# Optimization experiments

Hardware: AMD Instinct MI355X
Metric: run time of the kernel (lower is better)

Reference implementation:

```python
import jax, jax.numpy as jnp
import numpy as np

N_NODES = 50000
N_EDGES = 800000
IN_CH = 128
HID = 64
HEADS = 4
OUT_CH = 1
NEG_SLOPE = 0.2  # PyG GATConv default


def setup_inputs() -> dict:
    key = jax.random.key(0)
    ks = jax.random.split(key, 16)
    s = 0.1
    x = jax.random.normal(ks[0], (N_NODES, IN_CH), dtype=jnp.float32)
    edge_index = jax.random.randint(ks[1], (2, N_EDGES), 0, N_NODES, dtype=jnp.int64)
    # GATConv 1: in=128 -> 64 per head, 4 heads, concat
    W1 = jax.random.normal(ks[2], (IN_CH, HEADS * HID), dtype=jnp.float32) * s
    att_src1 = jax.random.normal(ks[3], (HEADS, HID), dtype=jnp.float32) * s
    att_dst1 = jax.random.normal(ks[4], (HEADS, HID), dtype=jnp.float32) * s
    b1 = jnp.zeros((HEADS * HID,), dtype=jnp.float32)
    # GATConv 2: in=256 -> 64, 1 head, mean (concat=False)
    W2 = jax.random.normal(ks[5], (HEADS * HID, HID), dtype=jnp.float32) * s
    att_src2 = jax.random.normal(ks[6], (1, HID), dtype=jnp.float32) * s
    att_dst2 = jax.random.normal(ks[7], (1, HID), dtype=jnp.float32) * s
    b2 = jnp.zeros((HID,), dtype=jnp.float32)
    # MLP: Linear(128,64) -> ReLU -> Linear(64,1)
    mlp_w1 = jax.random.normal(ks[8], (2 * HID, HID), dtype=jnp.float32) * s
    mlp_b1 = jnp.zeros((HID,), dtype=jnp.float32)
    mlp_w2 = jax.random.normal(ks[9], (HID, OUT_CH), dtype=jnp.float32) * s
    mlp_b2 = jnp.zeros((OUT_CH,), dtype=jnp.float32)
    return dict(x=x, edge_index=edge_index, W1=W1, att_src1=att_src1,
                att_dst1=att_dst1, b1=b1, W2=W2, att_src2=att_src2,
                att_dst2=att_dst2, b2=b2, mlp_w1=mlp_w1, mlp_b1=mlp_b1,
                mlp_w2=mlp_w2, mlp_b2=mlp_b2)


def gat_layer(x, edge_index, W, att_src, att_dst, bias, heads, ch, concat):
    N = x.shape[0]
    # add self loops (PyG default add_self_loops=True)
    loop = jnp.arange(N, dtype=edge_index.dtype)
    src = jnp.concatenate([edge_index[0], loop])
    dst = jnp.concatenate([edge_index[1], loop])
    h = (x @ W).reshape(N, heads, ch)                      # [N,H,C]
    a_src = jnp.einsum('nhc,hc->nh', h, att_src)           # [N,H]
    a_dst = jnp.einsum('nhc,hc->nh', h, att_dst)
    logits = jax.nn.leaky_relu(a_src[src] + a_dst[dst], NEG_SLOPE)  # [E,H]
    # segment softmax over destination node
    m = jax.ops.segment_max(logits, dst, num_segments=N)
    e = jnp.exp(logits - m[dst])
    denom = jax.ops.segment_sum(e, dst, num_segments=N)
    alpha = e / denom[dst]                                 # [E,H]
    msg = alpha[:, :, None] * h[src]                       # [E,H,C]
    out = jax.ops.segment_sum(msg, dst, num_segments=N)    # [N,H,C]
    out = out.reshape(N, heads * ch) if concat else out.mean(axis=1)
    return out + bias


def reference(x, edge_index, W1, att_src1, att_dst1, b1,
              W2, att_src2, att_dst2, b2,
              mlp_w1, mlp_b1, mlp_w2, mlp_b2):
    # eval mode: dropouts are identity
    h = gat_layer(x, edge_index, W1, att_src1, att_dst1, b1, HEADS, HID, True)
    h = jax.nn.elu(h)
    h = gat_layer(h, edge_index, W2, att_src2, att_dst2, b2, 1, HID, False)
    u = h[edge_index[0]]                                   # [E,HID]
    v = h[edge_index[1]]
    ef = jnp.concatenate([u, v], axis=1)                   # [E,2*HID]
    hid = jax.nn.relu(ef @ mlp_w1 + mlp_b1)
    return hid @ mlp_w2 + mlp_b2                           # [E,OUT_CH]
```

## Files before the change

kernel.cpp:

```cpp
#include <hip/hip_runtime.h>
#include <hip/hip_bf16.h>
#include <math.h>

#define NN 50000
#define NE 800000
#define NB ((NN + 255) / 256)
#define NEG 0.2f

typedef __hip_bfloat16 bf16;
typedef __attribute__((ext_vector_type(8))) short s8v;
typedef __attribute__((ext_vector_type(4))) float f4v;

__device__ __forceinline__ float bf2f(unsigned short u) {
  union { unsigned int i; float f; } c;
  c.i = ((unsigned int)u) << 16;
  return c.f;
}
__device__ __forceinline__ float blo(unsigned int u) {
  union { unsigned int i; float f; } c;
  c.i = u << 16;
  return c.f;
}
__device__ __forceinline__ float bhi(unsigned int u) {
  union { unsigned int i; float f; } c;
  c.i = u & 0xffff0000u;
  return c.f;
}
__device__ __forceinline__ unsigned short f2b(float f) {
  bf16 b = __float2bfloat16(f);
  return __builtin_bit_cast(unsigned short, b);
}
__device__ __forceinline__ float lrelu(float t) { return (t > 0.f) ? t : NEG * t; }

__global__ void hist_k(const int* __restrict__ ei, int* __restrict__ counts) {
  int e = blockIdx.x * 256 + threadIdx.x;
  if (e >= NE) return;
  atomicAdd(&counts[ei[NE + e]], 1);
}

__global__ __launch_bounds__(256) void scan_bsum_k(const int* __restrict__ counts,
                                                   int* __restrict__ bsums) {
  __shared__ int wsum[4];
  int i = blockIdx.x * 256 + threadIdx.x;
  int v = (i < NN) ? counts[i] : 0;
#pragma unroll
  for (int off = 32; off; off >>= 1) v += __shfl_xor(v, off);
  if ((threadIdx.x & 63) == 0) wsum[threadIdx.x >> 6] = v;
  __syncthreads();
  if (threadIdx.x == 0) bsums[blockIdx.x] = wsum[0] + wsum[1] + wsum[2] + wsum[3];
}

__global__ __launch_bounds__(256) void scan_final_k(const int* __restrict__ counts,
                                                    const int* __restrict__ bsums,
                                                    int* __restrict__ offsets,
                                                    int* __restrict__ cursor) {
  __shared__ int s[256];
  __shared__ int wsum[4];
  __shared__ int bpref;
  int t = threadIdx.x;
  int bv = (t < NB && t < (int)blockIdx.x) ? bsums[t] : 0;
#pragma unroll
  for (int off = 32; off; off >>= 1) bv += __shfl_xor(bv, off);
  if ((t & 63) == 0) wsum[t >> 6] = bv;
  __syncthreads();
  if (t == 0) bpref = wsum[0] + wsum[1] + wsum[2] + wsum[3];
  int i = blockIdx.x * 256 + t;
  int v = (i < NN) ? counts[i] : 0;
  s[t] = v;
  __syncthreads();
  for (int off = 1; off < 256; off <<= 1) {
    int u = (t >= off) ? s[t - off] : 0;
    __syncthreads();
    s[t] += u;
    __syncthreads();
  }
  int excl = s[t] - v + bpref;
  if (i < NN) {
    offsets[i] = excl;
    cursor[i] = excl;
    if (i == NN - 1) offsets[NN] = excl + v;
  }
}

__global__ void scatter_k(const int* __restrict__ ei, int* __restrict__ cursor,
                          int2* __restrict__ csr) {
  int e = blockIdx.x * 256 + threadIdx.x;
  if (e >= NE) return;
  int s = ei[e], d = ei[NE + e];
  int pos = atomicAdd(&cursor[d], 1);
  csr[pos] = make_int2(s, e);
}

#define NX4 (NN * 32)
#define NW1 (256 * 128)
#define NW2 (64 * 256)
#define NPQ (128 * 64)
__global__ void conv_all_k(const float* __restrict__ x, const float* __restrict__ W1,
                           const float* __restrict__ W2, const float* __restrict__ mw1,
                           unsigned short* __restrict__ xb, unsigned short* __restrict__ w1t,
                           unsigned short* __restrict__ w2t, unsigned short* __restrict__ pqt) {
  int i = blockIdx.x * 256 + threadIdx.x;
  if (i < NX4) {
    float4 v = *(const float4*)(x + (size_t)i * 4);
    ushort4 o = {f2b(v.x), f2b(v.y), f2b(v.z), f2b(v.w)};
    *(ushort4*)(xb + (size_t)i * 4) = o;
    return;
  }
  i -= NX4;
  if (i < NW1) {
    int n = i >> 7, k = i & 127;
    w1t[i] = f2b(W1[(size_t)k * 256 + n]);
    return;
  }
  i -= NW1;
  if (i < NW2) {
    int n = i >> 8, k = i & 255;
    w2t[i] = f2b(W2[(size_t)k * 64 + n]);
    return;
  }
  i -= NW2;
  if (i < NPQ) {
    int n = i >> 6, k = i & 63;
    float v = (n < 64) ? mw1[(size_t)k * 64 + n] : mw1[(size_t)(64 + k) * 64 + (n - 64)];
    pqt[i] = f2b(v);
  }
}

template <int DOTS>
__global__ __launch_bounds__(256) void mgemm_k(
    const unsigned short* __restrict__ A, int lda,
    const unsigned short* __restrict__ Bt, int ldb,
    unsigned short* __restrict__ C, int ldc,
    int M, int N, int K,
    const float* __restrict__ ws, const float* __restrict__ wd,
    float* __restrict__ as_, float* __restrict__ ad_, int H) {
  __shared__ unsigned short Asl[64][40];
  __shared__ unsigned short Btl[64][40];
  __shared__ float sdot[64], ddot[64];
  int bm = blockIdx.y * 64, bn = blockIdx.x * 64;
  int t = threadIdx.x;
  int wv = t >> 6, lane = t & 63;
  int wm = (wv >> 1) * 32, wn = (wv & 1) * 32;
  int l16 = lane & 15, lq = lane >> 4;
  if (DOTS && t < 64) { sdot[t] = 0.f; ddot[t] = 0.f; }
  f4v acc[2][2];
#pragma unroll
  for (int mi = 0; mi < 2; ++mi)
#pragma unroll
    for (int ni = 0; ni < 2; ++ni) {
      acc[mi][ni][0] = 0.f; acc[mi][ni][1] = 0.f;
      acc[mi][ni][2] = 0.f; acc[mi][ni][3] = 0.f;
    }
  int sr = t >> 2, sc = (t & 3) * 8;
  for (int k0 = 0; k0 < K; k0 += 32) {
    uint4 av = {0, 0, 0, 0};
    int gr = bm + sr;
    if (gr < M) av = *(const uint4*)(A + (size_t)gr * lda + k0 + sc);
    *(uint4*)&Asl[sr][sc] = av;
    uint4 bv = *(const uint4*)(Bt + (size_t)(bn + sr) * ldb + k0 + sc);
    *(uint4*)&Btl[sr][sc] = bv;
    __syncthreads();
    s8v af[2], bfv[2];
#pragma unroll
    for (int mi = 0; mi < 2; ++mi)
      af[mi] = *(const s8v*)&Asl[wm + mi * 16 + l16][lq * 8];
#pragma unroll
    for (int ni = 0; ni < 2; ++ni)
      bfv[ni] = *(const s8v*)&Btl[wn + ni * 16 + l16][lq * 8];
#pragma unroll
    for (int mi = 0; mi < 2; ++mi)
#pragma unroll
      for (int ni = 0; ni < 2; ++ni)
        acc[mi][ni] = __builtin_amdgcn_mfma_f32_16x16x32_bf16(
            af[mi], bfv[ni], acc[mi][ni], 0, 0, 0);
    __syncthreads();
  }
#pragma unroll
  for (int mi = 0; mi < 2; ++mi)
#pragma unroll
    for (int rr = 0; rr < 4; ++rr) {
      int row = bm + wm + mi * 16 + lq * 4 + rr;
      if (row < M) {
#pragma unroll
        for (int ni = 0; ni < 2; ++ni) {
          int col = bn + wn + ni * 16 + l16;
          C[(size_t)row * ldc + col] = f2b(acc[mi][ni][rr]);
        }
      }
    }
  if (DOTS) {
    int head = blockIdx.x;
    float ps[2][4], pd[2][4];
#pragma unroll
    for (int mi = 0; mi < 2; ++mi)
#pragma unroll
      for (int rr = 0; rr < 4; ++rr) {
        float s = 0.f, d = 0.f;
#pragma unroll
        for (int ni = 0; ni < 2; ++ni) {
          int col = wn + ni * 16 + l16;
          s += acc[mi][ni][rr] * ws[head * 64 + col];
          d += acc[mi][ni][rr] * wd[head * 64 + col];
        }
        ps[mi][rr] = s;
        pd[mi][rr] = d;
      }
#pragma unroll
    for (int off = 1; off < 16; off <<= 1)
#pragma unroll
      for (int mi = 0; mi < 2; ++mi)
#pragma unroll
        for (int rr = 0; rr < 4; ++rr) {
          ps[mi][rr] += __shfl_xor(ps[mi][rr], off);
          pd[mi][rr] += __shfl_xor(pd[mi][rr], off);
        }
    if (l16 == 0) {
#pragma unroll
      for (int mi = 0; mi < 2; ++mi)
#pragma unroll
        for (int rr = 0; rr < 4; ++rr) {
          int rl = wm + mi * 16 + lq * 4 + rr;
          atomicAdd(&sdot[rl], ps[mi][rr]);
          atomicAdd(&ddot[rl], pd[mi][rr]);
        }
    }
    __syncthreads();
    if (t < 64 && bm + t < M) {
      as_[(size_t)(bm + t) * H + head] = sdot[t];
      ad_[(size_t)(bm + t) * H + head] = ddot[t];
    }
  }
}

__global__ __launch_bounds__(256) void gat_agg4_k(
    const int* __restrict__ offsets, const int2* __restrict__ csr,
    const unsigned short* __restrict__ h, const float* __restrict__ as_,
    const float* __restrict__ ad_, const float* __restrict__ bias,
    unsigned short* __restrict__ out) {
  __shared__ float exs[4][64][4];
  __shared__ int srcs[4][64];
  int wvx = threadIdx.x >> 6, lane = threadIdx.x & 63;
  int n = blockIdx.x * 4 + wvx;
  int hd = lane >> 4;
  int beg = offsets[n], end = offsets[n + 1];
  float4 adn = *(const float4*)(ad_ + (size_t)n * 4);
  float4 asn = *(const float4*)(as_ + (size_t)n * 4);
  float es0 = __expf(lrelu(asn.x + adn.x));
  float es1 = __expf(lrelu(asn.y + adn.y));
  float es2 = __expf(lrelu(asn.z + adn.z));
  float es3 = __expf(lrelu(asn.w + adn.w));
  float d0 = es0, d1 = es1, d2 = es2, d3 = es3;
  float wself = (hd == 0) ? es0 : (hd == 1) ? es1 : (hd == 2) ? es2 : es3;
  uint2 sv = *(const uint2*)(h + (size_t)n * 256 + lane * 4);
  float2 a01, a23;
  a01.x = wself * blo(sv.x); a01.y = wself * bhi(sv.x);
  a23.x = wself * blo(sv.y); a23.y = wself * bhi(sv.y);
  for (int base = beg; base < end; base += 64) {
    int cnt = min(64, end - base);
    int src = 0;
    float e0 = 0.f, e1 = 0.f, e2 = 0.f, e3 = 0.f;
    if (lane < cnt) {
      src = csr[base + lane].x;
      float4 a4 = *(const float4*)(as_ + (size_t)src * 4);
      e0 = __expf(lrelu(a4.x + adn.x));
      e1 = __expf(lrelu(a4.y + adn.y));
      e2 = __expf(lrelu(a4.z + adn.z));
      e3 = __expf(lrelu(a4.w + adn.w));
    }
    float s0 = e0, s1 = e1, s2 = e2, s3 = e3;
#pragma unroll
    for (int off = 32; off; off >>= 1) {
      s0 += __shfl_xor(s0, off);
      s1 += __shfl_xor(s1, off);
      s2 += __shfl_xor(s2, off);
      s3 += __shfl_xor(s3, off);
    }
    d0 += s0; d1 += s1; d2 += s2; d3 += s3;
    float4 ex4 = {e0, e1, e2, e3};
    *(float4*)(&exs[wvx][lane][0]) = ex4;
    srcs[wvx][lane] = src;
    __builtin_amdgcn_wave_barrier();
    int e = 0;
    for (; e + 16 <= cnt; e += 16) {
      uint2 r[16];
#pragma unroll
      for (int j = 0; j < 16; ++j)
        r[j] = *(const uint2*)(h + (size_t)srcs[wvx][e + j] * 256 + lane * 4);
#pragma unroll
      for (int j = 0; j < 16; ++j) {
        float w = exs[wvx][e + j][hd];
        a01.x += w * blo(r[j].x); a01.y += w * bhi(r[j].x);
        a23.x += w * blo(r[j].y); a23.y += w * bhi(r[j].y);
      }
    }
    for (; e + 4 <= cnt; e += 4) {
      uint2 r[4];
#pragma unroll
      for (int j = 0; j < 4; ++j)
        r[j] = *(const uint2*)(h + (size_t)srcs[wvx][e + j] * 256 + lane * 4);
#pragma unroll
      for (int j = 0; j < 4; ++j) {
        float w = exs[wvx][e + j][hd];
        a01.x += w * blo(r[j].x); a01.y += w * bhi(r[j].x);
        a23.x += w * blo(r[j].y); a23.y += w * bhi(r[j].y);
      }
    }
    for (; e < cnt; ++e) {
      int si = srcs[wvx][e];
      float w = exs[wvx][e][hd];
      uint2 r = *(const uint2*)(h + (size_t)si * 256 + lane * 4);
      a01.x += w * blo(r.x); a01.y += w * bhi(r.x);
      a23.x += w * blo(r.y); a23.y += w * bhi(r.y);
    }
  }
  float myden = (hd == 0) ? d0 : (hd == 1) ? d1 : (hd == 2) ? d2 : d3;
  float inv = 1.f / myden;
  float4 b4 = *(const float4*)(bias + lane * 4);
  float4 res;
  res.x = a01.x * inv + b4.x;
  res.y = a01.y * inv + b4.y;
  res.z = a23.x * inv + b4.z;
  res.w = a23.y * inv + b4.w;
  res.x = (res.x > 0.f) ? res.x : (__expf(res.x) - 1.f);
  res.y = (res.y > 0.f) ? res.y : (__expf(res.y) - 1.f);
  res.z = (res.z > 0.f) ? res.z : (__expf(res.z) - 1.f);
  res.w = (res.w > 0.f) ? res.w : (__expf(res.w) - 1.f);
  ushort4 ov = {f2b(res.x), f2b(res.y), f2b(res.z), f2b(res.w)};
  *(ushort4*)(out + (size_t)n * 256 + lane * 4) = ov;
}

__global__ __launch_bounds__(256) void gat_agg1_k(
    const int* __restrict__ offsets, const int2* __restrict__ csr,
    const unsigned short* __restrict__ h, const float* __restrict__ as_,
    const float* __restrict__ ad_, const float* __restrict__ bias,
    unsigned short* __restrict__ out) {
  __shared__ float exs[4][64];
  __shared__ int srcs[4][64];
  int wvx = threadIdx.x >> 6, lane = threadIdx.x & 63;
  int n = blockIdx.x * 4 + wvx;
  int slot = lane >> 4, cp = lane & 15;
  int beg = offsets[n], end = offsets[n + 1];
  float adn = ad_[n];
  float eself = __expf(lrelu(as_[n] + adn));
  float den = eself;
  float2 a01 = {0.f, 0.f}, a23 = {0.f, 0.f};
  if (slot == 0) {
    uint2 sv = *(const uint2*)(h + (size_t)n * 64 + cp * 4);
    a01.x = eself * blo(sv.x); a01.y = eself * bhi(sv.x);
    a23.x = eself * blo(sv.y); a23.y = eself * bhi(sv.y);
  }
  for (int base = beg; base < end; base += 64) {
    int cnt = min(64, end - base);
    int src = 0;
    float ex = 0.f;
    if (lane < cnt) {
      src = csr[base + lane].x;
      ex = __expf(lrelu(as_[src] + adn));
    }
    float s = ex;
#pragma unroll
    for (int off = 32; off; off >>= 1) s += __shfl_xor(s, off);
    den += s;
    exs[wvx][lane] = ex;
    srcs[wvx][lane] = src;
    __builtin_amdgcn_wave_barrier();
    int i = slot;
    for (; i + 12 < cnt; i += 16) {
      uint2 r[4];
      int i0 = i, i1 = i + 4, i2 = i + 8, i3 = i + 12;
      r[0] = *(const uint2*)(h + (size_t)srcs[wvx][i0] * 64 + cp * 4);
      r[1] = *(const uint2*)(h + (size_t)srcs[wvx][i1] * 64 + cp * 4);
      r[2] = *(const uint2*)(h + (size_t)srcs[wvx][i2] * 64 + cp * 4);
      r[3] = *(const uint2*)(h + (size_t)srcs[wvx][i3] * 64 + cp * 4);
      float w0 = exs[wvx][i0], w1 = exs[wvx][i1], w2 = exs[wvx][i2], w3 = exs[wvx][i3];
      a01.x += w0 * blo(r[0].x); a01.y += w0 * bhi(r[0].x);
      a23.x += w0 * blo(r[0].y); a23.y += w0 * bhi(r[0].y);
      a01.x += w1 * blo(r[1].x); a01.y += w1 * bhi(r[1].x);
      a23.x += w1 * blo(r[1].y); a23.y += w1 * bhi(r[1].y);
      a01.x += w2 * blo(r[2].x); a01.y += w2 * bhi(r[2].x);
      a23.x += w2 * blo(r[2].y); a23.y += w2 * bhi(r[2].y);
      a01.x += w3 * blo(r[3].x); a01.y += w3 * bhi(r[3].x);
      a23.x += w3 * blo(r[3].y); a23.y += w3 * bhi(r[3].y);
    }
    for (; i < cnt; i += 4) {
      int si = srcs[wvx][i];
      float w = exs[wvx][i];
      uint2 r = *(const uint2*)(h + (size_t)si * 64 + cp * 4);
      a01.x += w * blo(r.x); a01.y += w * bhi(r.x);
      a23.x += w * blo(r.y); a23.y += w * bhi(r.y);
    }
  }
#pragma unroll
  for (int off = 16; off <= 32; off <<= 1) {
    a01.x += __shfl_xor(a01.x, off);
    a01.y += __shfl_xor(a01.y, off);
    a23.x += __shfl_xor(a23.x, off);
    a23.y += __shfl_xor(a23.y, off);
  }
  if (slot == 0) {
    float inv = 1.f / den;
    float4 b4 = *(const float4*)(bias + cp * 4);
    ushort4 ov;
    ov.x = f2b(a01.x * inv + b4.x);
    ov.y = f2b(a01.y * inv + b4.y);
    ov.z = f2b(a23.x * inv + b4.z);
    ov.w = f2b(a23.y * inv + b4.w);
    *(ushort4*)(out + (size_t)n * 64 + cp * 4) = ov;
  }
}

__global__ __launch_bounds__(256) void edge_out_k(
    const int* __restrict__ offsets, const int2* __restrict__ csr,
    const unsigned short* __restrict__ pq,
    const float* __restrict__ mb1, const float* __restrict__ w2,
    const float* __restrict__ mb2, float* __restrict__ out) {
  int wvx = threadIdx.x >> 6, lane = threadIdx.x & 63;
  int n = blockIdx.x * 4 + wvx;
  int slot = lane >> 4, cp = lane & 15;
  int beg = offsets[n], end = offsets[n + 1];
  ushort4 qv = *(const ushort4*)(pq + (size_t)n * 128 + 64 + cp * 4);
  float4 base4 = *(const float4*)(mb1 + cp * 4);
  base4.x += bf2f(qv.x); base4.y += bf2f(qv.y);
  base4.z += bf2f(qv.z); base4.w += bf2f(qv.w);
  float4 w4 = *(const float4*)(w2 + cp * 4);
  float b2v = mb2[0];
  for (int base = beg; base < end; base += 4) {
    int i = base + slot;
    int2 se = {0, 0};
    bool ok = (i < end);
    if (ok) se = csr[i];
    float r = 0.f;
    if (ok) {
      ushort4 pv = *(const ushort4*)(pq + (size_t)se.x * 128 + cp * 4);
      float v0 = fmaxf(bf2f(pv.x) + base4.x, 0.f);
      float v1 = fmaxf(bf2f(pv.y) + base4.y, 0.f);
      float v2 = fmaxf(bf2f(pv.z) + base4.z, 0.f);
      float v3 = fmaxf(bf2f(pv.w) + base4.w, 0.f);
      r = v0 * w4.x + v1 * w4.y + v2 * w4.z + v3 * w4.w;
    }
    r += __shfl_xor(r, 8);
    r += __shfl_xor(r, 4);
    r += __shfl_xor(r, 2);
    r += __shfl_xor(r, 1);
    if (cp == 0 && ok) out[se.y] = r + b2v;
  }
}

extern "C" void kernel_launch(void* const* d_in, const int* in_sizes, int n_in,
                              void* d_out, int out_size, void* d_ws, size_t ws_size,
                              hipStream_t stream) {
  const float* x = (const float*)d_in[0];
  const int* ei = (const int*)d_in[1];
  const float* W1 = (const float*)d_in[2];
  const float* as1w = (const float*)d_in[3];
  const float* ad1w = (const float*)d_in[4];
  const float* b1 = (const float*)d_in[5];
  const float* W2 = (const float*)d_in[6];
  const float* as2w = (const float*)d_in[7];
  const float* ad2w = (const float*)d_in[8];
  const float* b2 = (const float*)d_in[9];
  const float* mw1 = (const float*)d_in[10];
  const float* mb1 = (const float*)d_in[11];
  const float* mw2 = (const float*)d_in[12];
  const float* mb2 = (const float*)d_in[13];
  float* out = (float*)d_out;

  char* ws = (char*)d_ws;
  size_t o = 0;
  auto alloc = [&](size_t bytes) {
    void* ptr = ws + o;
    o += (bytes + 255) & ~(size_t)255;
    return ptr;
  };
  int* counts = (int*)alloc((size_t)NN * 4);
  int* offsets = (int*)alloc((size_t)(NN + 1) * 4);
  int* cursor = (int*)alloc((size_t)NN * 4);
  int* bsums = (int*)alloc((size_t)NB * 4);
  int2* csr = (int2*)alloc((size_t)NE * 8);
  unsigned short* xb = (unsigned short*)alloc((size_t)NN * 128 * 2);
  unsigned short* w1t = (unsigned short*)alloc((size_t)256 * 128 * 2);
  unsigned short* w2t = (unsigned short*)alloc((size_t)64 * 256 * 2);
  unsigned short* pqt = (unsigned short*)alloc((size_t)128 * 64 * 2);
  unsigned short* h1b = (unsigned short*)alloc((size_t)NN * 256 * 2);
  float* a_s1 = (float*)alloc((size_t)NN * 4 * 4);
  float* a_d1 = (float*)alloc((size_t)NN * 4 * 4);
  unsigned short* x2b = (unsigned short*)alloc((size_t)NN * 256 * 2);
  unsigned short* yb = (unsigned short*)alloc((size_t)NN * 64 * 2);
  unsigned short* h2b = h1b;
  unsigned short* pq = h1b + (size_t)NN * 64;

  hipMemsetAsync(counts, 0, (size_t)NN * 4, stream);
  hist_k<<<(NE + 255) / 256, 256, 0, stream>>>(ei, counts);
  scan_bsum_k<<<NB, 256, 0, stream>>>(counts, bsums);
  scan_final_k<<<NB, 256, 0, stream>>>(counts, bsums, offsets, cursor);
  scatter_k<<<(NE + 255) / 256, 256, 0, stream>>>(ei, cursor, csr);

  conv_all_k<<<(NX4 + NW1 + NW2 + NPQ + 255) / 256, 256, 0, stream>>>(
      x, W1, W2, mw1, xb, w1t, w2t, pqt);

  int gy = (NN + 63) / 64;
  mgemm_k<1><<<dim3(4, gy), 256, 0, stream>>>(xb, 128, w1t, 128, h1b, 256,
                                              NN, 256, 128, as1w, ad1w, a_s1, a_d1, 4);
  gat_agg4_k<<<NN / 4, 256, 0, stream>>>(offsets, csr, h1b, a_s1, a_d1, b1, x2b);

  mgemm_k<1><<<dim3(1, gy), 256, 0, stream>>>(x2b, 256, w2t, 256, h2b, 64,
                                              NN, 64, 256, as2w, ad2w, a_s1, a_d1, 1);
  gat_agg1_k<<<NN / 4, 256, 0, stream>>>(offsets, csr, h2b, a_s1, a_d1, b2, yb);

  mgemm_k<0><<<dim3(2, gy), 256, 0, stream>>>(yb, 64, pqt, 64, pq, 128,
                                              NN, 128, 64, nullptr, nullptr,
                                              nullptr, nullptr, 0);

  edge_out_k<<<NN / 4, 256, 0, stream>>>(offsets, csr, pq, mb1, mw2, mb2, out);
}
```

Measured before the change: 302.4 us.

## Fuse histogram with conversion, fold MLP projection into agg1, retune agg4 unroll

Merges the edge histogram and the bf16 conversion kernels into a single launch. The second GAT aggregation now computes the per-node P/Q MLP projection directly from a shared-memory copy of its output, which removes a GEMM launch and the yb intermediate round trip. The layer-1 aggregation gather loop goes from a 16/4 unroll to an 8-wide unroll with the weight loads hoisted. This cuts launches and memory traffic, but each wave now reads 16KB of weights per node from cache and does scalar FMAs instead of matrix-core work.

Measured after the change: 362.7 us. +19.9%, slower.

```diff
diff --git a/kernel.cpp b/kernel.cpp
--- a/kernel.cpp
+++ b/kernel.cpp
@@ -6,6 +6,7 @@
 #define NE 800000
 #define NB ((NN + 255) / 256)
 #define NEG 0.2f
+#define NHB ((NE + 255) / 256)
 
 typedef __hip_bfloat16 bf16;
 typedef __attribute__((ext_vector_type(8))) short s8v;
@@ -32,10 +33,46 @@
 }
 __device__ __forceinline__ float lrelu(float t) { return (t > 0.f) ? t : NEG * t; }
 
-__global__ void hist_k(const int* __restrict__ ei, int* __restrict__ counts) {
-  int e = blockIdx.x * 256 + threadIdx.x;
-  if (e >= NE) return;
-  atomicAdd(&counts[ei[NE + e]], 1);
+#define NX4 (NN * 32)
+#define NW1 (256 * 128)
+#define NW2 (64 * 256)
+#define NPQ (128 * 64)
+__global__ void prep_k(const int* __restrict__ ei, int* __restrict__ counts,
+                       const float* __restrict__ x, const float* __restrict__ W1,
+                       const float* __restrict__ W2, const float* __restrict__ mw1,
+                       unsigned short* __restrict__ xb, unsigned short* __restrict__ w1t,
+                       unsigned short* __restrict__ w2t, unsigned short* __restrict__ pqt) {
+  int b = blockIdx.x;
+  if (b < NHB) {
+    int e = b * 256 + threadIdx.x;
+    if (e < NE) atomicAdd(&counts[ei[NE + e]], 1);
+    return;
+  }
+  int i = (b - NHB) * 256 + threadIdx.x;
+  if (i < NX4) {
+    float4 v = *(const float4*)(x + (size_t)i * 4);
+    ushort4 o = {f2b(v.x), f2b(v.y), f2b(v.z), f2b(v.w)};
+    *(ushort4*)(xb + (size_t)i * 4) = o;
+    return;
+  }
+  i -= NX4;
+  if (i < NW1) {
+    int n = i >> 7, k = i & 127;
+    w1t[i] = f2b(W1[(size_t)k * 256 + n]);
+    return;
+  }
+  i -= NW1;
+  if (i < NW2) {
+    int n = i >> 8, k = i & 255;
+    w2t[i] = f2b(W2[(size_t)k * 64 + n]);
+    return;
+  }
+  i -= NW2;
+  if (i < NPQ) {
+    int n = i >> 6, k = i & 63;
+    float v = (n < 64) ? mw1[(size_t)k * 64 + n] : mw1[(size_t)(64 + k) * 64 + (n - 64)];
+    pqt[i] = f2b(v);
+  }
 }
 
 __global__ __launch_bounds__(256) void scan_bsum_k(const int* __restrict__ counts,
@@ -89,41 +126,6 @@
   int s = ei[e], d = ei[NE + e];
   int pos = atomicAdd(&cursor[d], 1);
   csr[pos] = make_int2(s, e);
-}
-
-#define NX4 (NN * 32)
-#define NW1 (256 * 128)
-#define NW2 (64 * 256)
-#define NPQ (128 * 64)
-__global__ void conv_all_k(const float* __restrict__ x, const float* __restrict__ W1,
-                           const float* __restrict__ W2, const float* __restrict__ mw1,
-                           unsigned short* __restrict__ xb, unsigned short* __restrict__ w1t,
-                           unsigned short* __restrict__ w2t, unsigned short* __restrict__ pqt) {
-  int i = blockIdx.x * 256 + threadIdx.x;
-  if (i < NX4) {
-    float4 v = *(const float4*)(x + (size_t)i * 4);
-    ushort4 o = {f2b(v.x), f2b(v.y), f2b(v.z), f2b(v.w)};
-    *(ushort4*)(xb + (size_t)i * 4) = o;
-    return;
-  }
-  i -= NX4;
-  if (i < NW1) {
-    int n = i >> 7, k = i & 127;
-    w1t[i] = f2b(W1[(size_t)k * 256 + n]);
-    return;
-  }
-  i -= NW1;
-  if (i < NW2) {
-    int n = i >> 8, k = i & 255;
-    w2t[i] = f2b(W2[(size_t)k * 64 + n]);
-    return;
-  }
-  i -= NW2;
-  if (i < NPQ) {
-    int n = i >> 6, k = i & 63;
-    float v = (n < 64) ? mw1[(size_t)k * 64 + n] : mw1[(size_t)(64 + k) * 64 + (n - 64)];
-    pqt[i] = f2b(v);
-  }
 }
 
 template <int DOTS>
@@ -281,28 +283,19 @@
     srcs[wvx][lane] = src;
     __builtin_amdgcn_wave_barrier();
     int e = 0;
-    for (; e + 16 <= cnt; e += 16) {
-      uint2 r[16];
-#pragma unroll
-      for (int j = 0; j < 16; ++j)
-        r[j] = *(const uint2*)(h + (size_t)srcs[wvx][e + j] * 256 + lane * 4);
-#pragma unroll
-      for (int j = 0; j < 16; ++j) {
-        float w = exs[wvx][e + j][hd];
-        a01.x += w * blo(r[j].x); a01.y += w * bhi(r[j].x);
-        a23.x += w * blo(r[j].y); a23.y += w * bhi(r[j].y);
+    for (; e + 8 <= cnt; e += 8) {
+      uint2 r[8];
+      float w[8];
+#pragma unroll
+      for (int j = 0; j < 8; ++j) {
+        int si = srcs[wvx][e + j];
+        w[j] = exs[wvx][e + j][hd];
+        r[j] = *(const uint2*)(h + (size_t)si * 256 + lane * 4);
       }
-    }
-    for (; e + 4 <= cnt; e += 4) {
-      uint2 r[4];
-#pragma unroll
-      for (int j = 0; j < 4; ++j)
-        r[j] = *(const uint2*)(h + (size_t)srcs[wvx][e + j] * 256 + lane * 4);
-#pragma unroll
-      for (int j = 0; j < 4; ++j) {
-        float w = exs[wvx][e + j][hd];
-        a01.x += w * blo(r[j].x); a01.y += w * bhi(r[j].x);
-        a23.x += w * blo(r[j].y); a23.y += w * bhi(r[j].y);
+#pragma unroll
+      for (int j = 0; j < 8; ++j) {
+        a01.x += w[j] * blo(r[j].x); a01.y += w[j] * bhi(r[j].x);
+        a23.x += w[j] * blo(r[j].y); a23.y += w[j] * bhi(r[j].y);
       }
     }
     for (; e < cnt; ++e) {
@@ -333,9 +326,10 @@
     const int* __restrict__ offsets, const int2* __restrict__ csr,
     const unsigned short* __restrict__ h, const float* __restrict__ as_,
     const float* __restrict__ ad_, const float* __restrict__ bias,
-    unsigned short* __restrict__ out) {
+    const unsigned short* __restrict__ pqt, unsigned short* __restrict__ pqo) {
   __shared__ float exs[4][64];
   __shared__ int srcs[4][64];
+  __shared__ float ych[4][64];
   int wvx = threadIdx.x >> 6, lane = threadIdx.x & 63;
   int n = blockIdx.x * 4 + wvx;
   int slot = lane >> 4, cp = lane & 15;
@@ -400,13 +394,30 @@
   if (slot == 0) {
     float inv = 1.f / den;
     float4 b4 = *(const float4*)(bias + cp * 4);
-    ushort4 ov;
-    ov.x = f2b(a01.x * inv + b4.x);
-    ov.y = f2b(a01.y * inv + b4.y);
-    ov.z = f2b(a23.x * inv + b4.z);
-    ov.w = f2b(a23.y * inv + b4.w);
-    *(ushort4*)(out + (size_t)n * 64 + cp * 4) = ov;
-  }
+    float4 yv;
+    yv.x = a01.x * inv + b4.x;
+    yv.y = a01.y * inv + b4.y;
+    yv.z = a23.x * inv + b4.z;
+    yv.w = a23.y * inv + b4.w;
+    *(float4*)(&ych[wvx][cp * 4]) = yv;
+  }
+  __builtin_amdgcn_wave_barrier();
+  float accp = 0.f, accq = 0.f;
+  const unsigned short* wp = pqt + (size_t)lane * 64;
+  const unsigned short* wq = pqt + (size_t)(lane + 64) * 64;
+#pragma unroll
+  for (int k = 0; k < 64; k += 8) {
+    uint4 wpv = *(const uint4*)(wp + k);
+    uint4 wqv = *(const uint4*)(wq + k);
+    float4 y0 = *(const float4*)(&ych[wvx][k]);
+    float4 y1 = *(const float4*)(&ych[wvx][k + 4]);
+    accp += y0.x * blo(wpv.x) + y0.y * bhi(wpv.x) + y0.z * blo(wpv.y) + y0.w * bhi(wpv.y)
+          + y1.x * blo(wpv.z) + y1.y * bhi(wpv.z) + y1.z * blo(wpv.w) + y1.w * bhi(wpv.w);
+    accq += y0.x * blo(wqv.x) + y0.y * bhi(wqv.x) + y0.z * blo(wqv.y) + y0.w * bhi(wqv.y)
+          + y1.x * blo(wqv.z) + y1.y * bhi(wqv.z) + y1.z * blo(wqv.w) + y1.w * bhi(wqv.w);
+  }
+  pqo[(size_t)n * 128 + lane] = f2b(accp);
+  pqo[(size_t)n * 128 + 64 + lane] = f2b(accq);
 }
 
 __global__ __launch_bounds__(256) void edge_out_k(
@@ -485,18 +496,15 @@
   float* a_s1 = (float*)alloc((size_t)NN * 4 * 4);
   float* a_d1 = (float*)alloc((size_t)NN * 4 * 4);
   unsigned short* x2b = (unsigned short*)alloc((size_t)NN * 256 * 2);
-  unsigned short* yb = (unsigned short*)alloc((size_t)NN * 64 * 2);
   unsigned short* h2b = h1b;
   unsigned short* pq = h1b + (size_t)NN * 64;
 
   hipMemsetAsync(counts, 0, (size_t)NN * 4, stream);
-  hist_k<<<(NE + 255) / 256, 256, 0, stream>>>(ei, counts);
+  prep_k<<<NHB + (NX4 + NW1 + NW2 + NPQ + 255) / 256, 256, 0, stream>>>(
+      ei, counts, x, W1, W2, mw1, xb, w1t, w2t, pqt);
   scan_bsum_k<<<NB, 256, 0, stream>>>(counts, bsums);
   scan_final_k<<<NB, 256, 0, stream>>>(counts, bsums, offsets, cursor);
   scatter_k<<<(NE + 255) / 256, 256, 0, stream>>>(ei, cursor, csr);
-
-  conv_all_k<<<(NX4 + NW1 + NW2 + NPQ + 255) / 256, 256, 0, stream>>>(
-      x, W1, W2, mw1, xb, w1t, w2t, pqt);
 
   int gy = (NN + 63) / 64;
   mgemm_k<1><<<dim3(4, gy), 256, 0, stream>>>(xb, 128, w1t, 128, h1b, 256,
@@ -505,11 +513,7 @@
 
   mgemm_k<1><<<dim3(1, gy), 256, 0, stream>>>(x2b, 256, w2t, 256, h2b, 64,
                                               NN, 64, 256, as2w, ad2w, a_s1, a_d1, 1);
-  gat_agg1_k<<<NN / 4, 256, 0, stream>>>(offsets, csr, h2b, a_s1, a_d1, b2, yb);
-
-  mgemm_k<0><<<dim3(2, gy), 256, 0, stream>>>(yb, 64, pqt, 64, pq, 128,
-                                              NN, 128, 64, nullptr, nullptr,
-                                              nullptr, nullptr, 0);
+  gat_agg1_k<<<NN / 4, 256, 0, stream>>>(offsets, csr, h2b, a_s1, a_d1, b2, pqt, pq);
 
   edge_out_k<<<NN / 4, 256, 0, stream>>>(offsets, csr, pq, mb1, mw2, mb2, out);
 }
```
